# Kernel optimization log

Hardware: AMD Instinct MI355X
Metric: run time of the kernel (lower is better)

Reference implementation:

```python
import jax, jax.numpy as jnp
import numpy as np

B = 4096
INPUT = 1024
HIDDEN = 2048
D_INNER = 2 * HIDDEN      # expand=2
DT_RANK = HIDDEN // 16    # 128
D_STATE = 16
LN_EPS = 1e-5


def setup_inputs() -> dict:
    key = jax.random.key(0)
    ks = jax.random.split(key, 12)
    s = lambda fan_in: 1.0 / np.sqrt(fan_in)
    inp = {
        "x": jax.random.normal(ks[0], (B, INPUT), jnp.float32),
        "h": jax.random.normal(ks[1], (B, HIDDEN), jnp.float32),
        # in_proj: Linear(input_size, 2*d_inner, bias=False)
        "W_in": jax.random.uniform(ks[2], (2 * D_INNER, INPUT), jnp.float32, -s(INPUT), s(INPUT)),
        # state_proj: Linear(hidden, d_inner, bias=False)
        "W_state": jax.random.uniform(ks[3], (D_INNER, HIDDEN), jnp.float32, -s(HIDDEN), s(HIDDEN)),
        # x_proj: Linear(d_inner, dt_rank + 2*d_state, bias=False)
        "W_xproj": jax.random.uniform(ks[4], (DT_RANK + 2 * D_STATE, D_INNER), jnp.float32, -s(D_INNER), s(D_INNER)),
        # dt_proj: Linear(dt_rank, d_inner, bias=True), weight ~ U(-dt_rank^-0.5, dt_rank^-0.5)
        "W_dt": jax.random.uniform(ks[5], (D_INNER, DT_RANK), jnp.float32, -s(DT_RANK), s(DT_RANK)),
        "b_dt": jnp.log(jnp.expm1(jnp.exp(jax.random.uniform(ks[6], (D_INNER,), jnp.float32)
                                           * (np.log(0.1) - np.log(0.001)) + np.log(0.001)))),
        # A_log = log(arange(1, d_state+1)) repeated over d_inner (unused in single-step math)
        "A_log": jnp.broadcast_to(jnp.log(jnp.arange(1, D_STATE + 1, dtype=jnp.float32)), (D_INNER, D_STATE)),
        "D": jnp.ones((D_INNER,), jnp.float32),
        # out_proj: Linear(d_inner, hidden, bias=False)
        "W_out": jax.random.uniform(ks[7], (HIDDEN, D_INNER), jnp.float32, -s(D_INNER), s(D_INNER)),
        # LayerNorm(hidden)
        "gamma": jnp.ones((HIDDEN,), jnp.float32),
        "beta": jnp.zeros((HIDDEN,), jnp.float32),
    }
    return inp


def _layernorm(x, gamma, beta):
    mu = jnp.mean(x, axis=-1, keepdims=True)
    var = jnp.mean(jnp.square(x - mu), axis=-1, keepdims=True)
    return (x - mu) * jax.lax.rsqrt(var + LN_EPS) * gamma + beta


def reference(x, h, W_in, W_state, W_xproj, W_dt, b_dt, A_log, D, W_out, gamma, beta):
    # in_proj and split into x branch / gate z
    xz = x @ W_in.T                               # [B, 2*d_inner]
    x_br, z = jnp.split(xz, 2, axis=-1)
    # add projected previous hidden state, then SiLU
    x_br = jax.nn.silu(x_br + h @ W_state.T)      # [B, d_inner]
    # x_proj -> (dt, B_mat, C)
    x_dbl = x_br @ W_xproj.T                      # [B, dt_rank + 2*d_state]
    dt_lo = x_dbl[:, :DT_RANK]
    B_mat = x_dbl[:, DT_RANK:DT_RANK + D_STATE]   # [B, d_state]
    C_mat = x_dbl[:, DT_RANK + D_STATE:]          # [B, d_state]
    dt = jax.nn.softplus(dt_lo @ W_dt.T + b_dt)   # [B, d_inner]
    # ssm_out[b,d] = sum_n dt[b,d]*B[b,n]*x_br[b,d]*C[b,n] + D[d]*x_br[b,d]
    bc = jnp.sum(B_mat * C_mat, axis=-1, keepdims=True)  # [B, 1]
    ssm_out = dt * x_br * bc + D * x_br           # [B, d_inner]
    # gate, output projection, residual, layernorm
    y = ssm_out * jax.nn.silu(z)
    h_new = y @ W_out.T + h
    return _layernorm(h_new, gamma, beta)
```

## Files before the change

kernel.cpp:

```cpp
#include <hip/hip_runtime.h>
#include <hip/hip_bf16.h>
#include <cstdint>
#include <cstddef>

typedef unsigned short u16;
typedef __bf16 bf16x8 __attribute__((ext_vector_type(8)));
typedef float f32x4 __attribute__((ext_vector_type(4)));

#define B_ROWS 4096
#define N_HIDDEN 2048
#define DT_RANK 128

static __device__ __forceinline__ u16 f2bf(float f) {
  unsigned u = __float_as_uint(f);
  u += 0x7FFFu + ((u >> 16) & 1u);
  return (u16)(u >> 16);
}
static __device__ __forceinline__ float bf2f(u16 b) {
  return __uint_as_float(((unsigned)b) << 16);
}
static __device__ __forceinline__ float siluf(float v) {
  return v / (1.0f + __expf(-v));
}
static __device__ __forceinline__ float softplusf(float v) {
  return v > 15.0f ? v : log1pf(__expf(v));
}
static __device__ __forceinline__ void async16(void* lds, const void* g) {
  __builtin_amdgcn_global_load_lds((const __attribute__((address_space(1))) void*)g,
                                   (__attribute__((address_space(3))) void*)lds, 16, 0, 0);
}

__global__ void cvt_bf16_kernel(const float* __restrict__ in, u16* __restrict__ out, int n4) {
  int i = blockIdx.x * blockDim.x + threadIdx.x;
  const int stride = gridDim.x * blockDim.x;
  for (; i < n4; i += stride) {
    float4 f = ((const float4*)in)[i];
    ushort4 o;
    o.x = f2bf(f.x); o.y = f2bf(f.y); o.z = f2bf(f.z); o.w = f2bf(f.w);
    ((ushort4*)out)[i] = o;
  }
}

__global__ void cvt_rows_kernel(const float* __restrict__ src, u16* __restrict__ dst,
                                int rl4, int dstride) {
  const int row = blockIdx.x;
  const float4* s = (const float4*)(src + (size_t)row * (rl4 * 4));
  ushort4* d = (ushort4*)(dst + (size_t)row * dstride);
  for (int c = threadIdx.x; c < rl4; c += blockDim.x) {
    float4 f = s[c];
    ushort4 o;
    o.x = f2bf(f.x); o.y = f2bf(f.y); o.z = f2bf(f.z); o.w = f2bf(f.w);
    d[c] = o;
  }
}

template <int NN, int KK, int LDA, int LDB, int EPI>
__global__ __launch_bounds__(512, 1)
void gemm8(const u16* __restrict__ A, const u16* __restrict__ Bw,
           float* __restrict__ outf, u16* __restrict__ outb, long long zstride)
{
  extern __shared__ u16 lds[];
  u16* ldsA = lds;
  u16* ldsB = lds + 32768;
  constexpr int NT = KK / 64;

  const int t = threadIdx.x;
  const int lane = t & 63, w = t >> 6;
  const int wr = w >> 2, wc = w & 3;
  const int r = lane & 15;
  const int q4 = lane >> 4;

  const int gx = gridDim.x;
  const int nwg = gx * gridDim.y;
  const int bid = blockIdx.y * gx + blockIdx.x;
  const int cpx = nwg >> 3;
  const int swz = (bid & 7) * cpx + (bid >> 3);
  const int n0 = (swz % gx) * 256;
  const int m0 = (swz / gx) * 256;
  const int koff = blockIdx.z * KK;

  f32x4 acc[8][4] = {};

  auto stA = [&](int buf, int half, int k0) {
#pragma unroll
    for (int i = 0; i < 2; ++i) {
      const int ii = w * 2 + i;
      const int c = ii * 64 + lane;
      const int row = c >> 3;
      const int ch = (c & 7) ^ (row & 7);
      async16(ldsA + (buf * 2 + half) * 8192 + ii * 512,
              A + (size_t)(m0 + half * 128 + row) * LDA + (koff + k0 + ch * 8));
    }
  };
  auto stB = [&](int buf, int half, int k0) {
#pragma unroll
    for (int i = 0; i < 2; ++i) {
      const int ii = w * 2 + i;
      const int c = ii * 64 + lane;
      const int row = c >> 3;
      const int ch = (c & 7) ^ (row & 7);
      async16(ldsB + (buf * 2 + half) * 8192 + ii * 512,
              Bw + (size_t)(n0 + half * 128 + row) * LDB + (koff + k0 + ch * 8));
    }
  };

  const int lrB0 = (wc & 1) * 64;
  const int aSlotHalf = wr;
  const int bSlotHalf = wc >> 1;

  auto ldA = [&](int buf, int lr, int kki) -> bf16x8 {
    const int tt = kki * 4 + q4;
    return *(const bf16x8*)(ldsA + (size_t)((buf * 2 + aSlotHalf) * 8192 + lr * 64 + ((tt ^ (lr & 7)) << 3)));
  };
  auto ldB = [&](int buf, int lr, int kki) -> bf16x8 {
    const int tt = kki * 4 + q4;
    return *(const bf16x8*)(ldsB + (size_t)((buf * 2 + bSlotHalf) * 8192 + lr * 64 + ((tt ^ (lr & 7)) << 3)));
  };

  stA(0, 0, 0); stA(0, 1, 0); stB(0, 0, 0); stB(0, 1, 0);
  stA(1, 0, 64);
  asm volatile("s_waitcnt vmcnt(2)" ::: "memory");
  asm volatile("" ::: "memory");
  __builtin_amdgcn_s_barrier();
  asm volatile("" ::: "memory");

  int cur = 0;
  for (int j = 0; j < NT; ++j) {
    const int nxt = cur ^ 1;
    bf16x8 fa[4], fah[4], fb0[4], fb1[4];
#pragma unroll
    for (int f = 0; f < 4; ++f) fa[f] = ldA(cur, f * 16 + r, 0);
#pragma unroll
    for (int g = 0; g < 4; ++g) fb0[g] = ldB(cur, lrB0 + g * 16 + r, 0);
    if (j + 1 < NT) stA(nxt, 1, (j + 1) * 64);
    asm volatile("" ::: "memory");
    __builtin_amdgcn_s_barrier();
    asm volatile("s_waitcnt lgkmcnt(0)" ::: "memory");
    __builtin_amdgcn_s_setprio(1);
#pragma unroll
    for (int f = 0; f < 4; ++f)
#pragma unroll
      for (int g = 0; g < 4; ++g)
        acc[f][g] = __builtin_amdgcn_mfma_f32_16x16x32_bf16(fa[f], fb0[g], acc[f][g], 0, 0, 0);
    __builtin_amdgcn_s_setprio(0);
    asm volatile("" ::: "memory");
    __builtin_amdgcn_s_barrier();
    asm volatile("" ::: "memory");
#pragma unroll
    for (int f = 0; f < 4; ++f) fah[f] = ldA(cur, 64 + f * 16 + r, 0);
#pragma unroll
    for (int g = 0; g < 4; ++g) fb1[g] = ldB(cur, lrB0 + g * 16 + r, 1);
    if (j + 1 < NT) stB(nxt, 0, (j + 1) * 64);
    asm volatile("" ::: "memory");
    __builtin_amdgcn_s_barrier();
    asm volatile("s_waitcnt lgkmcnt(0)" ::: "memory");
    __builtin_amdgcn_s_setprio(1);
#pragma unroll
    for (int f = 0; f < 4; ++f)
#pragma unroll
      for (int g = 0; g < 4; ++g)
        acc[4 + f][g] = __builtin_amdgcn_mfma_f32_16x16x32_bf16(fah[f], fb0[g], acc[4 + f][g], 0, 0, 0);
    __builtin_amdgcn_s_setprio(0);
    asm volatile("" ::: "memory");
    __builtin_amdgcn_s_barrier();
    asm volatile("" ::: "memory");
#pragma unroll
    for (int f = 0; f < 4; ++f) fa[f] = ldA(cur, f * 16 + r, 1);
#pragma unroll
    for (int f = 0; f < 4; ++f) fah[f] = ldA(cur, 64 + f * 16 + r, 1);
    if (j + 1 < NT) stB(nxt, 1, (j + 1) * 64);
    asm volatile("" ::: "memory");
    __builtin_amdgcn_s_barrier();
    asm volatile("s_waitcnt lgkmcnt(0)" ::: "memory");
    __builtin_amdgcn_s_setprio(1);
#pragma unroll
    for (int f = 0; f < 4; ++f)
#pragma unroll
      for (int g = 0; g < 4; ++g)
        acc[f][g] = __builtin_amdgcn_mfma_f32_16x16x32_bf16(fa[f], fb1[g], acc[f][g], 0, 0, 0);
    __builtin_amdgcn_s_setprio(0);
    asm volatile("" ::: "memory");
    __builtin_amdgcn_s_barrier();
    asm volatile("" ::: "memory");
    if (j + 2 < NT) stA(cur, 0, (j + 2) * 64);
    asm volatile("" ::: "memory");
    __builtin_amdgcn_s_barrier();
    __builtin_amdgcn_s_setprio(1);
#pragma unroll
    for (int f = 0; f < 4; ++f)
#pragma unroll
      for (int g = 0; g < 4; ++g)
        acc[4 + f][g] = __builtin_amdgcn_mfma_f32_16x16x32_bf16(fah[f], fb1[g], acc[4 + f][g], 0, 0, 0);
    __builtin_amdgcn_s_setprio(0);
    if (j + 2 < NT) { asm volatile("s_waitcnt vmcnt(2)" ::: "memory"); }
    else            { asm volatile("s_waitcnt vmcnt(0)" ::: "memory"); }
    asm volatile("" ::: "memory");
    __builtin_amdgcn_s_barrier();
    asm volatile("" ::: "memory");
    cur = nxt;
  }

  const int rr = q4 * 4;
  const int cc = r;
  float* of = outf ? (outf + (size_t)blockIdx.z * zstride) : nullptr;
#pragma unroll
  for (int f8 = 0; f8 < 8; ++f8) {
#pragma unroll
    for (int g = 0; g < 4; ++g) {
#pragma unroll
      for (int tt = 0; tt < 4; ++tt) {
        const int grow = m0 + wr * 128 + f8 * 16 + rr + tt;
        const int gcol = n0 + wc * 64 + g * 16 + cc;
        const float v = acc[f8][g][tt];
        if constexpr (EPI == 0) {
          outb[(size_t)grow * NN + gcol] = f2bf(siluf(v));
        } else {
          of[(size_t)grow * NN + gcol] = v;
        }
      }
    }
  }
}

template <int NN, int KK, int LDA, int EPI>
__global__ __launch_bounds__(256)
void gemm_bt(const u16* __restrict__ A, const u16* __restrict__ Bw,
             float* __restrict__ outf, u16* __restrict__ outb,
             const float* __restrict__ aux1, const float* __restrict__ aux2,
             const float* __restrict__ aux3,
             const u16* __restrict__ xaux, const u16* __restrict__ saux)
{
  constexpr int BM = 128, BK = 64;
  __shared__ alignas(16) u16 As[2][BM * BK];
  __shared__ alignas(16) u16 Bs[2][BM * BK];
  const int t = threadIdx.x;
  const int lane = t & 63, w = t >> 6;
  const int m0 = blockIdx.y * BM, n0 = blockIdx.x * BM;
  const int mw = (w >> 1) * 64, nw = (w & 1) * 64;
  const int r = lane & 15;
  const int kq = (lane >> 4) * 8;

  f32x4 acc[4][4] = {};

  auto stage = [&](int buf, int k0) {
#pragma unroll
    for (int i = 0; i < 4; ++i) {
      const int slot0 = (w * 4 + i) * 64;
      const int s = slot0 + lane;
      const int row = s >> 3, cs = (s & 7) * 8;
      async16(&As[buf][slot0 * 8], A + (size_t)(m0 + row) * LDA + k0 + cs);
      async16(&Bs[buf][slot0 * 8], Bw + (size_t)(n0 + row) * KK + k0 + cs);
    }
  };

  stage(0, 0);
  asm volatile("s_waitcnt vmcnt(0)" ::: "memory");
  __syncthreads();
  int cur = 0;

  for (int k0 = 0; k0 < KK; k0 += BK) {
    if (k0 + BK < KK) stage(cur ^ 1, k0 + BK);
#pragma unroll
    for (int kk = 0; kk < BK; kk += 32) {
      bf16x8 af[4], bb[4];
#pragma unroll
      for (int f = 0; f < 4; ++f)
        af[f] = *(const bf16x8*)(&As[cur][(mw + f * 16 + r) * BK + kk + kq]);
#pragma unroll
      for (int f = 0; f < 4; ++f)
        bb[f] = *(const bf16x8*)(&Bs[cur][(nw + f * 16 + r) * BK + kk + kq]);
#pragma unroll
      for (int fm = 0; fm < 4; ++fm)
#pragma unroll
        for (int fn = 0; fn < 4; ++fn)
          acc[fm][fn] = __builtin_amdgcn_mfma_f32_16x16x32_bf16(af[fm], bb[fn], acc[fm][fn], 0, 0, 0);
    }
    asm volatile("s_waitcnt vmcnt(0)" ::: "memory");
    __syncthreads();
    cur ^= 1;
  }

  const int rr = (lane >> 4) * 4;
  const int cc = lane & 15;
#pragma unroll
  for (int fm = 0; fm < 4; ++fm) {
#pragma unroll
    for (int fn = 0; fn < 4; ++fn) {
#pragma unroll
      for (int tt = 0; tt < 4; ++tt) {
        const int grow = m0 + mw + fm * 16 + rr + tt;
        const int gcol = n0 + nw + fn * 16 + cc;
        float v = acc[fm][fn][tt];
        if constexpr (EPI == 2) {
          float dt = softplusf(v + aux1[gcol]);
          float xv = bf2f(xaux[(size_t)grow * NN + gcol]);
          float sv = bf2f(saux[(size_t)grow * NN + gcol]);
          float yv = xv * (dt * aux2[grow] + aux3[gcol]) * sv;
          outb[(size_t)grow * NN + gcol] = f2bf(yv);
        } else {
          outf[(size_t)grow * NN + gcol] = v;
        }
      }
    }
  }
}

__global__ __launch_bounds__(256)
void gemm_xproj(const u16* __restrict__ A, const u16* __restrict__ Bw,
                float* __restrict__ part)
{
  constexpr int BK = 64;
  __shared__ alignas(16) u16 As[64 * BK];
  __shared__ alignas(16) u16 Bs[160 * BK];
  const int t = threadIdx.x, lane = t & 63, w = t >> 6;
  const int m0 = blockIdx.x * 64;
  const int kz = blockIdx.y;
  const int r = lane & 15, kq = (lane >> 4) * 8;
  f32x4 acc[10] = {};
  for (int kt = 0; kt < 1024; kt += BK) {
    const int k0 = kz * 1024 + kt;
#pragma unroll
    for (int i = 0; i < 2; ++i) {
      const int slot0 = (w * 2 + i) * 64;
      const int s = slot0 + lane;
      async16(As + slot0 * 8, A + (size_t)(m0 + (s >> 3)) * 4096 + k0 + (s & 7) * 8);
    }
#pragma unroll
    for (int i = 0; i < 5; ++i) {
      const int slot0 = (w * 5 + i) * 64;
      const int s = slot0 + lane;
      async16(Bs + slot0 * 8, Bw + (size_t)(s >> 3) * 4096 + k0 + (s & 7) * 8);
    }
    asm volatile("s_waitcnt vmcnt(0)" ::: "memory");
    __syncthreads();
#pragma unroll
    for (int kk = 0; kk < BK; kk += 32) {
      bf16x8 af = *(const bf16x8*)(As + (w * 16 + r) * BK + kk + kq);
#pragma unroll
      for (int fn = 0; fn < 10; ++fn) {
        bf16x8 bb = *(const bf16x8*)(Bs + (fn * 16 + r) * BK + kk + kq);
        acc[fn] = __builtin_amdgcn_mfma_f32_16x16x32_bf16(af, bb, acc[fn], 0, 0, 0);
      }
    }
    __syncthreads();
  }
  float* o = part + (size_t)kz * B_ROWS * 160;
  const int rr = (lane >> 4) * 4, cc = lane & 15;
#pragma unroll
  for (int fn = 0; fn < 10; ++fn)
#pragma unroll
    for (int tt = 0; tt < 4; ++tt)
      o[(size_t)(m0 + w * 16 + rr + tt) * 160 + fn * 16 + cc] = acc[fn][tt];
}

__global__ __launch_bounds__(192)
void xdbl_reduce(const float* __restrict__ part, u16* __restrict__ dtlo,
                 float* __restrict__ bc)
{
  const int row = blockIdx.x, t = threadIdx.x;
  __shared__ float cvals[32];
  float v = 0.0f;
  if (t < 160) {
    const float* p = part + (size_t)row * 160 + t;
#pragma unroll
    for (int z = 0; z < 4; ++z) v += p[(size_t)z * B_ROWS * 160];
  }
  if (t < DT_RANK) dtlo[(size_t)row * DT_RANK + t] = f2bf(v);
  if (t >= DT_RANK && t < 160) cvals[t - DT_RANK] = v;
  __syncthreads();
  if (t == 0) {
    float s = 0.0f;
#pragma unroll
    for (int j = 0; j < 16; ++j) s += cvals[j] * cvals[j + 16];
    bc[row] = s;
  }
}

__global__ __launch_bounds__(256)
void ln_kernel(const float* __restrict__ p0, const float* __restrict__ p1,
               const float* __restrict__ hh, const float* __restrict__ gamma,
               const float* __restrict__ beta, float* __restrict__ out)
{
  const int row = blockIdx.x, t = threadIdx.x;
  __shared__ float red[4];
  const float4* x0 = (const float4*)(p0 + (size_t)row * N_HIDDEN);
  const float4* x1 = (const float4*)(p1 + (size_t)row * N_HIDDEN);
  const float4* xh = (const float4*)(hh + (size_t)row * N_HIDDEN);
  float4 a, b;
  {
    float4 u = x0[t], v = x1[t], w = xh[t];
    a.x = u.x + v.x + w.x; a.y = u.y + v.y + w.y; a.z = u.z + v.z + w.z; a.w = u.w + v.w + w.w;
    u = x0[t + 256]; v = x1[t + 256]; w = xh[t + 256];
    b.x = u.x + v.x + w.x; b.y = u.y + v.y + w.y; b.z = u.z + v.z + w.z; b.w = u.w + v.w + w.w;
  }
  float s = ((a.x + a.y) + (a.z + a.w)) + ((b.x + b.y) + (b.z + b.w));
#pragma unroll
  for (int m = 32; m; m >>= 1) s += __shfl_xor(s, m);
  if ((t & 63) == 0) red[t >> 6] = s;
  __syncthreads();
  s = (red[0] + red[1]) + (red[2] + red[3]);
  const float mu = s * (1.0f / N_HIDDEN);
  float dx0 = a.x - mu, dx1 = a.y - mu, dx2 = a.z - mu, dx3 = a.w - mu;
  float dy0 = b.x - mu, dy1 = b.y - mu, dy2 = b.z - mu, dy3 = b.w - mu;
  float q = ((dx0 * dx0 + dx1 * dx1) + (dx2 * dx2 + dx3 * dx3)) +
            ((dy0 * dy0 + dy1 * dy1) + (dy2 * dy2 + dy3 * dy3));
  __syncthreads();
#pragma unroll
  for (int m = 32; m; m >>= 1) q += __shfl_xor(q, m);
  if ((t & 63) == 0) red[t >> 6] = q;
  __syncthreads();
  q = (red[0] + red[1]) + (red[2] + red[3]);
  const float inv = rsqrtf(q * (1.0f / N_HIDDEN) + 1e-5f);
  const float4 ga = ((const float4*)gamma)[t], gb = ((const float4*)gamma)[t + 256];
  const float4 ba = ((const float4*)beta)[t], bbv = ((const float4*)beta)[t + 256];
  float4 o0, o1;
  o0.x = dx0 * inv * ga.x + ba.x;
  o0.y = dx1 * inv * ga.y + ba.y;
  o0.z = dx2 * inv * ga.z + ba.z;
  o0.w = dx3 * inv * ga.w + ba.w;
  o1.x = dy0 * inv * gb.x + bbv.x;
  o1.y = dy1 * inv * gb.y + bbv.y;
  o1.z = dy2 * inv * gb.z + bbv.z;
  o1.w = dy3 * inv * gb.w + bbv.w;
  float4* o4 = (float4*)(out + (size_t)row * N_HIDDEN);
  o4[t] = o0;
  o4[t + 256] = o1;
}

extern "C" void kernel_launch(void* const* d_in, const int* in_sizes, int n_in,
                              void* d_out, int out_size, void* d_ws, size_t ws_size,
                              hipStream_t stream) {
  const float* x     = (const float*)d_in[0];
  const float* h     = (const float*)d_in[1];
  const float* W_in  = (const float*)d_in[2];
  const float* W_st  = (const float*)d_in[3];
  const float* W_xp  = (const float*)d_in[4];
  const float* W_dt  = (const float*)d_in[5];
  const float* b_dt  = (const float*)d_in[6];
  const float* Dv    = (const float*)d_in[8];
  const float* W_out = (const float*)d_in[9];
  const float* gamma = (const float*)d_in[10];
  const float* beta  = (const float*)d_in[11];
  float* out = (float*)d_out;
  (void)in_sizes; (void)n_in; (void)out_size; (void)ws_size;

  char* ws = (char*)d_ws;
  size_t o = 0;
  auto alloc = [&](size_t bytes) { char* p = ws + o; o += bytes; return p; };
  u16* Acat    = (u16*)alloc((size_t)4096 * 3072 * 2);
  u16* Wcat    = (u16*)alloc((size_t)4096 * 3072 * 2);
  u16* Wz_bf   = (u16*)alloc((size_t)4096 * 1024 * 2);
  u16* Wxp_bf  = (u16*)alloc((size_t)160 * 4096 * 2);
  u16* Wdt_bf  = (u16*)alloc((size_t)4096 * 128 * 2);
  u16* Wout_bf = (u16*)alloc((size_t)2048 * 4096 * 2);
  u16* xbr_bf  = (u16*)alloc((size_t)4096 * 4096 * 2);
  u16* sz_bf   = (u16*)alloc((size_t)4096 * 4096 * 2);
  float* part  = (float*)alloc((size_t)4 * 4096 * 160 * 4);
  u16* dtlo_bf = (u16*)alloc((size_t)4096 * 128 * 2);
  float* bc    = (float*)alloc((size_t)4096 * 4);
  u16* y_bf = (u16*)Acat;
  float* p0 = (float*)xbr_bf;
  float* p1 = p0 + (size_t)4096 * 2048;

  auto cvt = [&](const float* src, u16* dst, size_t n) {
    int n4 = (int)(n / 4);
    int blocks = (n4 + 255) / 256;
    if (blocks > 2048) blocks = 2048;
    cvt_bf16_kernel<<<blocks, 256, 0, stream>>>(src, dst, n4);
  };
  cvt_rows_kernel<<<4096, 256, 0, stream>>>(x,    Acat,        256, 3072);
  cvt_rows_kernel<<<4096, 256, 0, stream>>>(h,    Acat + 1024, 512, 3072);
  cvt_rows_kernel<<<4096, 256, 0, stream>>>(W_in, Wcat,        256, 3072);
  cvt_rows_kernel<<<4096, 256, 0, stream>>>(W_st, Wcat + 1024, 512, 3072);
  cvt(W_in + (size_t)4096 * 1024, Wz_bf, (size_t)4096 * 1024);
  cvt(W_xp, Wxp_bf, (size_t)160 * 4096);
  cvt(W_dt, Wdt_bf, (size_t)4096 * 128);
  cvt(W_out, Wout_bf, (size_t)2048 * 4096);

  gemm8<4096, 3072, 3072, 3072, 0><<<dim3(16, 16, 1), 512, 131072, stream>>>(
      Acat, Wcat, nullptr, xbr_bf, 0);
  gemm8<4096, 1024, 3072, 1024, 0><<<dim3(16, 16, 1), 512, 131072, stream>>>(
      Acat, Wz_bf, nullptr, sz_bf, 0);
  gemm_xproj<<<dim3(64, 4), 256, 0, stream>>>(xbr_bf, Wxp_bf, part);
  xdbl_reduce<<<4096, 192, 0, stream>>>(part, dtlo_bf, bc);
  gemm_bt<4096, 128, 128, 2><<<dim3(32, 32), 256, 0, stream>>>(
      dtlo_bf, Wdt_bf, nullptr, y_bf, b_dt, bc, Dv, xbr_bf, sz_bf);
  gemm8<2048, 2048, 4096, 4096, 1><<<dim3(8, 16, 2), 512, 131072, stream>>>(
      y_bf, Wout_bf, p0, nullptr, (long long)4096 * 2048);
  ln_kernel<<<4096, 256, 0, stream>>>(p0, p1, h, gamma, beta, out);
}
```

Baseline: 376.8 us.

## Restructure gemm8 main loop into quadrant-interleaved software pipeline

Rewrites the 256x256 bf16 GEMM inner loop so each wave owns interleaved 16-row and 16-column fragments. Each K-tile is split into four quadrant MFMA phases, and the last quadrant is carried into the next iteration to overlap with the following LDS reads. Waits now use partial lgkmcnt/vmcnt counts instead of full drains, and launch bounds now request 2 blocks per CU. The aim is to hide LDS and global load latency behind MFMA work. It costs more live fragment registers, and the hand-tuned wait counts are fragile.

```diff
diff --git a/kernel.cpp b/kernel.cpp
--- a/kernel.cpp
+++ b/kernel.cpp
@@ -55,7 +55,7 @@
 }
 
 template <int NN, int KK, int LDA, int LDB, int EPI>
-__global__ __launch_bounds__(512, 1)
+__global__ __launch_bounds__(512, 2)
 void gemm8(const u16* __restrict__ A, const u16* __restrict__ Bw,
            float* __restrict__ outf, u16* __restrict__ outb, long long zstride)
 {
@@ -63,6 +63,7 @@
   u16* ldsA = lds;
   u16* ldsB = lds + 32768;
   constexpr int NT = KK / 64;
+  static_assert(NT >= 2, "need at least 2 K-tiles");
 
   const int t = threadIdx.x;
   const int lane = t & 63, w = t >> 6;
@@ -80,6 +81,7 @@
   const int koff = blockIdx.z * KK;
 
   f32x4 acc[8][4] = {};
+  bf16x8 a0[4][2], a1[4][2], b0[2][2], b1[2][2];
 
   auto stA = [&](int buf, int half, int k0) {
 #pragma unroll
@@ -104,114 +106,152 @@
     }
   };
 
-  const int lrB0 = (wc & 1) * 64;
-  const int aSlotHalf = wr;
-  const int bSlotHalf = wc >> 1;
-
-  auto ldA = [&](int buf, int lr, int kki) -> bf16x8 {
-    const int tt = kki * 4 + q4;
-    return *(const bf16x8*)(ldsA + (size_t)((buf * 2 + aSlotHalf) * 8192 + lr * 64 + ((tt ^ (lr & 7)) << 3)));
+  auto ldA = [&](int buf, int half, int lrow, int ks) -> bf16x8 {
+    const int tt = ks * 4 + q4;
+    return *(const bf16x8*)(ldsA + (size_t)((buf * 2 + half) * 8192 + lrow * 64 + ((tt ^ (lrow & 7)) << 3)));
   };
-  auto ldB = [&](int buf, int lr, int kki) -> bf16x8 {
-    const int tt = kki * 4 + q4;
-    return *(const bf16x8*)(ldsB + (size_t)((buf * 2 + bSlotHalf) * 8192 + lr * 64 + ((tt ^ (lr & 7)) << 3)));
+  auto ldB = [&](int buf, int half, int lrow, int ks) -> bf16x8 {
+    const int tt = ks * 4 + q4;
+    return *(const bf16x8*)(ldsB + (size_t)((buf * 2 + half) * 8192 + lrow * 64 + ((tt ^ (lrow & 7)) << 3)));
   };
 
-  stA(0, 0, 0); stA(0, 1, 0); stB(0, 0, 0); stB(0, 1, 0);
-  stA(1, 0, 64);
-  asm volatile("s_waitcnt vmcnt(2)" ::: "memory");
-  asm volatile("" ::: "memory");
+  stA(0, 0, 0); stB(0, 0, 0); stA(0, 1, 0); stB(0, 1, 0);
+  stA(1, 0, 64); stB(1, 0, 64);
+  asm volatile("s_waitcnt vmcnt(10)" ::: "memory");
   __builtin_amdgcn_s_barrier();
   asm volatile("" ::: "memory");
 
   int cur = 0;
   for (int j = 0; j < NT; ++j) {
     const int nxt = cur ^ 1;
-    bf16x8 fa[4], fah[4], fb0[4], fb1[4];
-#pragma unroll
-    for (int f = 0; f < 4; ++f) fa[f] = ldA(cur, f * 16 + r, 0);
-#pragma unroll
-    for (int g = 0; g < 4; ++g) fb0[g] = ldB(cur, lrB0 + g * 16 + r, 0);
+    const bool lastj = (j == NT - 1);
+
+#pragma unroll
+    for (int ii = 0; ii < 4; ++ii) {
+      const int lr = (2 * ii + wr) * 16 + r;
+      a0[ii][0] = ldA(cur, 0, lr, 0);
+      a0[ii][1] = ldA(cur, 0, lr, 1);
+    }
     if (j + 1 < NT) stA(nxt, 1, (j + 1) * 64);
+    asm volatile("" ::: "memory");
+    __builtin_amdgcn_s_barrier();
+    asm volatile("s_waitcnt lgkmcnt(8)" ::: "memory");
+    if (j > 0) {
+      __builtin_amdgcn_s_setprio(1);
+#pragma unroll
+      for (int ii = 0; ii < 4; ++ii)
+#pragma unroll
+        for (int gg = 0; gg < 2; ++gg) {
+          acc[4 + ii][2 + gg] = __builtin_amdgcn_mfma_f32_16x16x32_bf16(a1[ii][0], b1[gg][0], acc[4 + ii][2 + gg], 0, 0, 0);
+          acc[4 + ii][2 + gg] = __builtin_amdgcn_mfma_f32_16x16x32_bf16(a1[ii][1], b1[gg][1], acc[4 + ii][2 + gg], 0, 0, 0);
+        }
+      __builtin_amdgcn_s_setprio(0);
+    }
+    if (lastj) { asm volatile("s_waitcnt vmcnt(2)" ::: "memory"); }
+    else       { asm volatile("s_waitcnt vmcnt(8)" ::: "memory"); }
+    __builtin_amdgcn_s_barrier();
+    asm volatile("" ::: "memory");
+
+#pragma unroll
+    for (int gg = 0; gg < 2; ++gg) {
+      const int lrb = (wc + 4 * gg) * 16 + r;
+      b0[gg][0] = ldB(cur, 0, lrb, 0);
+      b0[gg][1] = ldB(cur, 0, lrb, 1);
+    }
+#pragma unroll
+    for (int ii = 0; ii < 4; ++ii) {
+      const int lr = (2 * ii + wr) * 16 + r;
+      a1[ii][0] = ldA(cur, 1, lr, 0);
+    }
+    if (j + 1 < NT) stB(nxt, 1, (j + 1) * 64);
+    asm volatile("" ::: "memory");
+    __builtin_amdgcn_s_barrier();
+    asm volatile("s_waitcnt lgkmcnt(4)" ::: "memory");
+    __builtin_amdgcn_s_setprio(1);
+#pragma unroll
+    for (int ii = 0; ii < 4; ++ii)
+#pragma unroll
+      for (int gg = 0; gg < 2; ++gg) {
+        acc[ii][gg] = __builtin_amdgcn_mfma_f32_16x16x32_bf16(a0[ii][0], b0[gg][0], acc[ii][gg], 0, 0, 0);
+        acc[ii][gg] = __builtin_amdgcn_mfma_f32_16x16x32_bf16(a0[ii][1], b0[gg][1], acc[ii][gg], 0, 0, 0);
+      }
+    __builtin_amdgcn_s_setprio(0);
+    if (lastj) { asm volatile("s_waitcnt vmcnt(0)" ::: "memory"); }
+    else       { asm volatile("s_waitcnt vmcnt(8)" ::: "memory"); }
+    __builtin_amdgcn_s_barrier();
+    asm volatile("" ::: "memory");
+
+#pragma unroll
+    for (int gg = 0; gg < 2; ++gg) {
+      const int lrb = (wc + 4 * gg) * 16 + r;
+      b1[gg][0] = ldB(cur, 1, lrb, 0);
+      b1[gg][1] = ldB(cur, 1, lrb, 1);
+    }
+#pragma unroll
+    for (int ii = 0; ii < 4; ++ii) {
+      const int lr = (2 * ii + wr) * 16 + r;
+      a1[ii][1] = ldA(cur, 1, lr, 1);
+    }
+    if (j + 2 < NT) stA(cur, 0, (j + 2) * 64);
+    asm volatile("" ::: "memory");
+    __builtin_amdgcn_s_barrier();
+    asm volatile("s_waitcnt lgkmcnt(4)" ::: "memory");
+    __builtin_amdgcn_s_setprio(1);
+#pragma unroll
+    for (int ii = 0; ii < 4; ++ii)
+#pragma unroll
+      for (int gg = 0; gg < 2; ++gg) {
+        acc[ii][2 + gg] = __builtin_amdgcn_mfma_f32_16x16x32_bf16(a0[ii][0], b1[gg][0], acc[ii][2 + gg], 0, 0, 0);
+        acc[ii][2 + gg] = __builtin_amdgcn_mfma_f32_16x16x32_bf16(a0[ii][1], b1[gg][1], acc[ii][2 + gg], 0, 0, 0);
+      }
+    __builtin_amdgcn_s_setprio(0);
+    asm volatile("" ::: "memory");
+    __builtin_amdgcn_s_barrier();
+    asm volatile("" ::: "memory");
+
+    if (j + 2 < NT) stB(cur, 0, (j + 2) * 64);
     asm volatile("" ::: "memory");
     __builtin_amdgcn_s_barrier();
     asm volatile("s_waitcnt lgkmcnt(0)" ::: "memory");
     __builtin_amdgcn_s_setprio(1);
 #pragma unroll
-    for (int f = 0; f < 4; ++f)
-#pragma unroll
-      for (int g = 0; g < 4; ++g)
-        acc[f][g] = __builtin_amdgcn_mfma_f32_16x16x32_bf16(fa[f], fb0[g], acc[f][g], 0, 0, 0);
+    for (int ii = 0; ii < 4; ++ii)
+#pragma unroll
+      for (int gg = 0; gg < 2; ++gg) {
+        acc[4 + ii][gg] = __builtin_amdgcn_mfma_f32_16x16x32_bf16(a1[ii][0], b0[gg][0], acc[4 + ii][gg], 0, 0, 0);
+        acc[4 + ii][gg] = __builtin_amdgcn_mfma_f32_16x16x32_bf16(a1[ii][1], b0[gg][1], acc[4 + ii][gg], 0, 0, 0);
+      }
     __builtin_amdgcn_s_setprio(0);
-    asm volatile("" ::: "memory");
-    __builtin_amdgcn_s_barrier();
-    asm volatile("" ::: "memory");
-#pragma unroll
-    for (int f = 0; f < 4; ++f) fah[f] = ldA(cur, 64 + f * 16 + r, 0);
-#pragma unroll
-    for (int g = 0; g < 4; ++g) fb1[g] = ldB(cur, lrB0 + g * 16 + r, 1);
-    if (j + 1 < NT) stB(nxt, 0, (j + 1) * 64);
-    asm volatile("" ::: "memory");
-    __builtin_amdgcn_s_barrier();
-    asm volatile("s_waitcnt lgkmcnt(0)" ::: "memory");
-    __builtin_amdgcn_s_setprio(1);
-#pragma unroll
-    for (int f = 0; f < 4; ++f)
-#pragma unroll
-      for (int g = 0; g < 4; ++g)
-        acc[4 + f][g] = __builtin_amdgcn_mfma_f32_16x16x32_bf16(fah[f], fb0[g], acc[4 + f][g], 0, 0, 0);
-    __builtin_amdgcn_s_setprio(0);
-    asm volatile("" ::: "memory");
-    __builtin_amdgcn_s_barrier();
-    asm volatile("" ::: "memory");
-#pragma unroll
-    for (int f = 0; f < 4; ++f) fa[f] = ldA(cur, f * 16 + r, 1);
-#pragma unroll
-    for (int f = 0; f < 4; ++f) fah[f] = ldA(cur, 64 + f * 16 + r, 1);
-    if (j + 1 < NT) stB(nxt, 1, (j + 1) * 64);
-    asm volatile("" ::: "memory");
-    __builtin_amdgcn_s_barrier();
-    asm volatile("s_waitcnt lgkmcnt(0)" ::: "memory");
-    __builtin_amdgcn_s_setprio(1);
-#pragma unroll
-    for (int f = 0; f < 4; ++f)
-#pragma unroll
-      for (int g = 0; g < 4; ++g)
-        acc[f][g] = __builtin_amdgcn_mfma_f32_16x16x32_bf16(fa[f], fb1[g], acc[f][g], 0, 0, 0);
-    __builtin_amdgcn_s_setprio(0);
-    asm volatile("" ::: "memory");
-    __builtin_amdgcn_s_barrier();
-    asm volatile("" ::: "memory");
-    if (j + 2 < NT) stA(cur, 0, (j + 2) * 64);
-    asm volatile("" ::: "memory");
-    __builtin_amdgcn_s_barrier();
-    __builtin_amdgcn_s_setprio(1);
-#pragma unroll
-    for (int f = 0; f < 4; ++f)
-#pragma unroll
-      for (int g = 0; g < 4; ++g)
-        acc[4 + f][g] = __builtin_amdgcn_mfma_f32_16x16x32_bf16(fah[f], fb1[g], acc[4 + f][g], 0, 0, 0);
-    __builtin_amdgcn_s_setprio(0);
-    if (j + 2 < NT) { asm volatile("s_waitcnt vmcnt(2)" ::: "memory"); }
-    else            { asm volatile("s_waitcnt vmcnt(0)" ::: "memory"); }
+    if (j + 1 < NT) {
+      if (j + 1 == NT - 1) { asm volatile("s_waitcnt vmcnt(6)" ::: "memory"); }
+      else                 { asm volatile("s_waitcnt vmcnt(10)" ::: "memory"); }
+    }
     asm volatile("" ::: "memory");
     __builtin_amdgcn_s_barrier();
     asm volatile("" ::: "memory");
     cur = nxt;
   }
 
-  const int rr = q4 * 4;
-  const int cc = r;
+  __builtin_amdgcn_s_setprio(1);
+#pragma unroll
+  for (int ii = 0; ii < 4; ++ii)
+#pragma unroll
+    for (int gg = 0; gg < 2; ++gg) {
+      acc[4 + ii][2 + gg] = __builtin_amdgcn_mfma_f32_16x16x32_bf16(a1[ii][0], b1[gg][0], acc[4 + ii][2 + gg], 0, 0, 0);
+      acc[4 + ii][2 + gg] = __builtin_amdgcn_mfma_f32_16x16x32_bf16(a1[ii][1], b1[gg][1], acc[4 + ii][2 + gg], 0, 0, 0);
+    }
+  __builtin_amdgcn_s_setprio(0);
+
   float* of = outf ? (outf + (size_t)blockIdx.z * zstride) : nullptr;
 #pragma unroll
-  for (int f8 = 0; f8 < 8; ++f8) {
+  for (int i = 0; i < 8; ++i) {
 #pragma unroll
     for (int g = 0; g < 4; ++g) {
 #pragma unroll
       for (int tt = 0; tt < 4; ++tt) {
-        const int grow = m0 + wr * 128 + f8 * 16 + rr + tt;
-        const int gcol = n0 + wc * 64 + g * 16 + cc;
-        const float v = acc[f8][g][tt];
+        const int grow = m0 + (2 * i + wr) * 16 + q4 * 4 + tt;
+        const int gcol = n0 + (wc + 4 * g) * 16 + r;
+        const float v = acc[i][g][tt];
         if constexpr (EPI == 0) {
           outb[(size_t)grow * NN + gcol] = f2bf(siluf(v));
         } else {
```

Measured after the change: 468.3 us. 24.3% more time.
